# Optimization experiments

Hardware: AMD Instinct MI355X
Metric: run time of the kernel (lower is better)

The kernel has to match this reference:

```python
import jax, jax.numpy as jnp
import numpy as np

N = 1_000_000   # voxels (stride-1: in grid == out grid)
C = 32          # channels
K = 27          # 3x3x3 kernel offsets
P = 600_000     # rulebook pairs per offset
BN_EPS = 1e-5


def setup_inputs() -> dict:
    key = jax.random.key(0)
    k1, k2, k3, k4 = jax.random.split(key, 4)
    x = jax.random.normal(k1, (N, C), dtype=jnp.float32)
    # He-style init for conv weights: fan_in = K * C
    W = jax.random.normal(k2, (K, C, C), dtype=jnp.float32) * (1.0 / np.sqrt(K * C))
    gamma = jnp.ones((C,), dtype=jnp.float32)
    beta = jnp.zeros((C,), dtype=jnp.float32)
    in_idx = jax.random.randint(k3, (K, P), 0, N, dtype=jnp.int32)
    out_idx = jax.random.randint(k4, (K, P), 0, N, dtype=jnp.int32)
    return {"x": x, "W": W, "gamma": gamma, "beta": beta,
            "in_idx": in_idx, "out_idx": out_idx}


def _sparse_conv(x, W, in_idx, out_idx):
    # Rulebook-driven sparse conv: for each kernel offset k, gather input
    # voxels, multiply by the offset's [C,C] weight, scatter-add to outputs.
    def step(acc, inputs):
        ii, oi, w = inputs                      # [P], [P], [C,C]
        acc = acc.at[oi].add(x[ii] @ w)          # gather -> GEMM -> scatter
        return acc, None
    out0 = jnp.zeros((x.shape[0], W.shape[-1]), dtype=x.dtype)
    out, _ = jax.lax.scan(step, out0, (in_idx, out_idx, W))
    return out


def reference(x, W, gamma, beta, in_idx, out_idx):
    y = _sparse_conv(x, W, in_idx, out_idx)      # [N, C]
    # BatchNorm (training-mode batch stats over all voxels, per channel)
    mean = jnp.mean(y, axis=0)
    var = jnp.var(y, axis=0)
    y = (y - mean) * jax.lax.rsqrt(var + BN_EPS) * gamma + beta
    # ReLU
    return jnp.maximum(y, 0.0)
```

## Files before the change

### kernel.cpp

```cpp
#include <hip/hip_runtime.h>

#define CH 32
#define KOFF 27
#define BN_EPS 1e-5f

typedef short bf16x8 __attribute__((ext_vector_type(8)));
typedef float f32x4 __attribute__((ext_vector_type(4)));

__device__ __forceinline__ unsigned short f2bf(float f) {
    unsigned u = __builtin_bit_cast(unsigned, f);
    u = (u + 0x7fffu + ((u >> 16) & 1u)) >> 16;
    return (unsigned short)u;
}
__device__ __forceinline__ float bf2f_lo(unsigned u) {
    return __builtin_bit_cast(float, u << 16);
}
__device__ __forceinline__ float bf2f_hi(unsigned u) {
    return __builtin_bit_cast(float, u & 0xffff0000u);
}

__global__ __launch_bounds__(256) void conv_pk_kernel(
    const float* __restrict__ x, const float* __restrict__ W,
    const int* __restrict__ in_idx, const int* __restrict__ out_idx,
    unsigned* __restrict__ ybf,
    int P, int tilesPerK, int tilesPerWave)
{
    const int k    = blockIdx.y;
    const int lane = threadIdx.x & 63;
    const int wv   = threadIdx.x >> 6;
    const int r16  = lane & 15;
    const int g    = lane >> 4;

    const float* Wk = W + k * CH * CH;
    bf16x8 b0, b1;
#pragma unroll
    for (int j = 0; j < 8; ++j) {
        int kk = g * 8 + j;
        b0[j] = (short)f2bf(Wk[kk * CH + 2 * r16]);
        b1[j] = (short)f2bf(Wk[kk * CH + 2 * r16 + 1]);
    }

    const int kP = k * P;
    int t0 = (blockIdx.x * 4 + wv) * tilesPerWave;
    int t1 = t0 + tilesPerWave;
    if (t1 > tilesPerK) t1 = tilesPerK;

    for (int t = t0; t < t1; ++t) {
        const int base = t * 16;
        int pi = base + r16;
        if (pi >= P) pi = P - 1;
        const int ii = in_idx[kP + pi];
        const float* xr = x + ii * CH + g * 8;
        f32x4 x0 = *(const f32x4*)xr;
        f32x4 x1 = *(const f32x4*)(xr + 4);
        bf16x8 a;
        a[0] = (short)f2bf(x0[0]); a[1] = (short)f2bf(x0[1]);
        a[2] = (short)f2bf(x0[2]); a[3] = (short)f2bf(x0[3]);
        a[4] = (short)f2bf(x1[0]); a[5] = (short)f2bf(x1[1]);
        a[6] = (short)f2bf(x1[2]); a[7] = (short)f2bf(x1[3]);

        f32x4 d0 = {0.f, 0.f, 0.f, 0.f};
        f32x4 d1 = {0.f, 0.f, 0.f, 0.f};
        d0 = __builtin_amdgcn_mfma_f32_16x16x32_bf16(a, b0, d0, 0, 0, 0);
        d1 = __builtin_amdgcn_mfma_f32_16x16x32_bf16(a, b1, d1, 0, 0, 0);

#pragma unroll
        for (int i = 0; i < 4; ++i) {
            int pr = base + g * 4 + i;
            if (pr < P) {
                int oi = out_idx[kP + pr];
                unsigned pk = (unsigned)f2bf(d0[i]) | ((unsigned)f2bf(d1[i]) << 16);
                unsigned* addr = ybf + (size_t)oi * (CH / 2) + r16;
                asm volatile("global_atomic_pk_add_bf16 %0, %1, off"
                             :: "v"(addr), "v"(pk) : "memory");
            }
        }
    }
}

__global__ __launch_bounds__(256) void stats_pk_kernel(
    const uint4* __restrict__ y4, float* __restrict__ stats, int n4)
{
    __shared__ float ls[CH], ls2[CH];
    if (threadIdx.x < CH) { ls[threadIdx.x] = 0.f; ls2[threadIdx.x] = 0.f; }
    __syncthreads();

    int tid = blockIdx.x * blockDim.x + threadIdx.x;
    int stride = gridDim.x * blockDim.x;
    float s[8] = {0,0,0,0,0,0,0,0}, q[8] = {0,0,0,0,0,0,0,0};
    for (int i = tid; i < n4; i += stride) {
        uint4 v = y4[i];
        float f0 = bf2f_lo(v.x), f1 = bf2f_hi(v.x);
        float f2 = bf2f_lo(v.y), f3 = bf2f_hi(v.y);
        float f4 = bf2f_lo(v.z), f5 = bf2f_hi(v.z);
        float f6 = bf2f_lo(v.w), f7 = bf2f_hi(v.w);
        s[0]+=f0; q[0]+=f0*f0; s[1]+=f1; q[1]+=f1*f1;
        s[2]+=f2; q[2]+=f2*f2; s[3]+=f3; q[3]+=f3*f3;
        s[4]+=f4; q[4]+=f4*f4; s[5]+=f5; q[5]+=f5*f5;
        s[6]+=f6; q[6]+=f6*f6; s[7]+=f7; q[7]+=f7*f7;
    }
    int c = (tid * 8) & (CH - 1);
#pragma unroll
    for (int j = 0; j < 8; ++j) {
        atomicAdd(&ls[c + j], s[j]);
        atomicAdd(&ls2[c + j], q[j]);
    }
    __syncthreads();
    if (threadIdx.x < CH) {
        atomicAdd(&stats[threadIdx.x], ls[threadIdx.x]);
        atomicAdd(&stats[CH + threadIdx.x], ls2[threadIdx.x]);
    }
}

__global__ __launch_bounds__(256) void bn_relu_pk_kernel(
    const uint4* __restrict__ y4, f32x4* __restrict__ out4,
    const float* __restrict__ stats,
    const float* __restrict__ gamma, const float* __restrict__ beta,
    float invN, int n4)
{
    __shared__ float sc[CH], bi[CH];
    if (threadIdx.x < CH) {
        int c = threadIdx.x;
        float mean = stats[c] * invN;
        float var  = stats[CH + c] * invN - mean * mean;
        float s = gamma[c] * rsqrtf(var + BN_EPS);
        sc[c] = s;
        bi[c] = beta[c] - mean * s;
    }
    __syncthreads();

    int tid = blockIdx.x * blockDim.x + threadIdx.x;
    int stride = gridDim.x * blockDim.x;
    for (int i = tid; i < n4; i += stride) {
        uint4 v = y4[i];
        int c = (i * 8) & (CH - 1);
        f32x4 o0, o1;
        o0[0] = fmaxf(bf2f_lo(v.x) * sc[c+0] + bi[c+0], 0.f);
        o0[1] = fmaxf(bf2f_hi(v.x) * sc[c+1] + bi[c+1], 0.f);
        o0[2] = fmaxf(bf2f_lo(v.y) * sc[c+2] + bi[c+2], 0.f);
        o0[3] = fmaxf(bf2f_hi(v.y) * sc[c+3] + bi[c+3], 0.f);
        o1[0] = fmaxf(bf2f_lo(v.z) * sc[c+4] + bi[c+4], 0.f);
        o1[1] = fmaxf(bf2f_hi(v.z) * sc[c+5] + bi[c+5], 0.f);
        o1[2] = fmaxf(bf2f_lo(v.w) * sc[c+6] + bi[c+6], 0.f);
        o1[3] = fmaxf(bf2f_hi(v.w) * sc[c+7] + bi[c+7], 0.f);
        out4[2 * i]     = o0;
        out4[2 * i + 1] = o1;
    }
}

__global__ __launch_bounds__(256) void conv_kernel(
    const float* __restrict__ x, const float* __restrict__ W,
    const int* __restrict__ in_idx, const int* __restrict__ out_idx,
    float* __restrict__ y, int P, int tilesPerK, int tilesPerWave)
{
    const int k    = blockIdx.y;
    const int lane = threadIdx.x & 63;
    const int wv   = threadIdx.x >> 6;
    const int r16  = lane & 15;
    const int g    = lane >> 4;

    const float* Wk = W + k * CH * CH;
    bf16x8 b0, b1;
#pragma unroll
    for (int j = 0; j < 8; ++j) {
        int kk = g * 8 + j;
        b0[j] = (short)f2bf(Wk[kk * CH + r16]);
        b1[j] = (short)f2bf(Wk[kk * CH + 16 + r16]);
    }

    const int kP = k * P;
    int t0 = (blockIdx.x * 4 + wv) * tilesPerWave;
    int t1 = t0 + tilesPerWave;
    if (t1 > tilesPerK) t1 = tilesPerK;

    for (int t = t0; t < t1; ++t) {
        const int base = t * 16;
        int pi = base + r16;
        if (pi >= P) pi = P - 1;
        const int ii = in_idx[kP + pi];
        const float* xr = x + ii * CH + g * 8;
        f32x4 x0 = *(const f32x4*)xr;
        f32x4 x1 = *(const f32x4*)(xr + 4);
        bf16x8 a;
        a[0] = (short)f2bf(x0[0]); a[1] = (short)f2bf(x0[1]);
        a[2] = (short)f2bf(x0[2]); a[3] = (short)f2bf(x0[3]);
        a[4] = (short)f2bf(x1[0]); a[5] = (short)f2bf(x1[1]);
        a[6] = (short)f2bf(x1[2]); a[7] = (short)f2bf(x1[3]);

        f32x4 d0 = {0.f, 0.f, 0.f, 0.f};
        f32x4 d1 = {0.f, 0.f, 0.f, 0.f};
        d0 = __builtin_amdgcn_mfma_f32_16x16x32_bf16(a, b0, d0, 0, 0, 0);
        d1 = __builtin_amdgcn_mfma_f32_16x16x32_bf16(a, b1, d1, 0, 0, 0);

#pragma unroll
        for (int i = 0; i < 4; ++i) {
            int pr = base + g * 4 + i;
            if (pr < P) {
                int oi = out_idx[kP + pr];
                atomicAdd(&y[oi * CH + r16], d0[i]);
                atomicAdd(&y[oi * CH + 16 + r16], d1[i]);
            }
        }
    }
}

__global__ __launch_bounds__(256) void stats_kernel(
    const f32x4* __restrict__ y4, float* __restrict__ stats, int n4)
{
    __shared__ float ls[CH], ls2[CH];
    if (threadIdx.x < CH) { ls[threadIdx.x] = 0.f; ls2[threadIdx.x] = 0.f; }
    __syncthreads();

    int tid = blockIdx.x * blockDim.x + threadIdx.x;
    int stride = gridDim.x * blockDim.x;
    float s0 = 0, s1 = 0, s2 = 0, s3 = 0;
    float q0 = 0, q1 = 0, q2 = 0, q3 = 0;
    for (int i = tid; i < n4; i += stride) {
        f32x4 v = y4[i];
        s0 += v[0]; q0 += v[0] * v[0];
        s1 += v[1]; q1 += v[1] * v[1];
        s2 += v[2]; q2 += v[2] * v[2];
        s3 += v[3]; q3 += v[3] * v[3];
    }
    int c = (tid * 4) & (CH - 1);
    atomicAdd(&ls[c + 0], s0); atomicAdd(&ls[c + 1], s1);
    atomicAdd(&ls[c + 2], s2); atomicAdd(&ls[c + 3], s3);
    atomicAdd(&ls2[c + 0], q0); atomicAdd(&ls2[c + 1], q1);
    atomicAdd(&ls2[c + 2], q2); atomicAdd(&ls2[c + 3], q3);
    __syncthreads();
    if (threadIdx.x < CH) {
        atomicAdd(&stats[threadIdx.x], ls[threadIdx.x]);
        atomicAdd(&stats[CH + threadIdx.x], ls2[threadIdx.x]);
    }
}

__global__ __launch_bounds__(256) void bn_relu_kernel(
    f32x4* __restrict__ y4, const float* __restrict__ stats,
    const float* __restrict__ gamma, const float* __restrict__ beta,
    float invN, int n4)
{
    __shared__ float sc[CH], bi[CH];
    if (threadIdx.x < CH) {
        int c = threadIdx.x;
        float mean = stats[c] * invN;
        float var  = stats[CH + c] * invN - mean * mean;
        float s = gamma[c] * rsqrtf(var + BN_EPS);
        sc[c] = s;
        bi[c] = beta[c] - mean * s;
    }
    __syncthreads();

    int tid = blockIdx.x * blockDim.x + threadIdx.x;
    int stride = gridDim.x * blockDim.x;
    for (int i = tid; i < n4; i += stride) {
        f32x4 v = y4[i];
        int c = (i * 4) & (CH - 1);
        f32x4 o;
        o[0] = fmaxf(v[0] * sc[c + 0] + bi[c + 0], 0.f);
        o[1] = fmaxf(v[1] * sc[c + 1] + bi[c + 1], 0.f);
        o[2] = fmaxf(v[2] * sc[c + 2] + bi[c + 2], 0.f);
        o[3] = fmaxf(v[3] * sc[c + 3] + bi[c + 3], 0.f);
        y4[i] = o;
    }
}

extern "C" void kernel_launch(void* const* d_in, const int* in_sizes, int n_in,
                              void* d_out, int out_size, void* d_ws, size_t ws_size,
                              hipStream_t stream)
{
    const float* x      = (const float*)d_in[0];
    const float* W      = (const float*)d_in[1];
    const float* gamma  = (const float*)d_in[2];
    const float* beta   = (const float*)d_in[3];
    const int*   in_idx = (const int*)d_in[4];
    const int*   out_idx= (const int*)d_in[5];

    const int P = in_sizes[4] / KOFF;
    const int N = in_sizes[0] / CH;

    const int tilesPerK = (P + 15) / 16;
    const int tilesPerWave = 8;
    const int blocksX = (tilesPerK + 4 * tilesPerWave - 1) / (4 * tilesPerWave);

    float* stats = (float*)d_ws;
    const size_t statsBytes = 256;
    const size_t ybfBytes = (size_t)N * CH * 2;

    if (ws_size >= statsBytes + ybfBytes) {
        unsigned* ybf = (unsigned*)((char*)d_ws + statsBytes);
        hipMemsetAsync(d_ws, 0, statsBytes + ybfBytes, stream);

        conv_pk_kernel<<<dim3(blocksX, KOFF), 256, 0, stream>>>(
            x, W, in_idx, out_idx, ybf, P, tilesPerK, tilesPerWave);

        const int n4 = (N * CH) / 8;
        stats_pk_kernel<<<1024, 256, 0, stream>>>((const uint4*)ybf, stats, n4);
        bn_relu_pk_kernel<<<2048, 256, 0, stream>>>(
            (const uint4*)ybf, (f32x4*)d_out, stats, gamma, beta,
            1.0f / (float)N, n4);
    } else {
        float* y = (float*)d_out;
        hipMemsetAsync(d_out, 0, (size_t)out_size * sizeof(float), stream);
        hipMemsetAsync(d_ws, 0, statsBytes, stream);

        conv_kernel<<<dim3(blocksX, KOFF), 256, 0, stream>>>(
            x, W, in_idx, out_idx, y, P, tilesPerK, tilesPerWave);

        const int n4 = out_size / 4;
        stats_kernel<<<1024, 256, 0, stream>>>((const f32x4*)d_out, stats, n4);
        bn_relu_kernel<<<2048, 256, 0, stream>>>((f32x4*)d_out, stats, gamma, beta,
                                                 1.0f / (float)N, n4);
    }
}
```

Baseline: 900.1 us.

## Accumulate conv output as packed 16-bit fixed-point via 64-bit integer atomics

The scatter-add no longer uses packed bf16 atomics. Each output value is quantized to 16-bit fixed point (scale 512), and four channels are packed into one u64 using a lane shuffle, so every output row takes 8 64-bit atomic adds instead of 16 32-bit ones. The stats and BN kernels decode the packed fields with borrow correction. This halves the number of atomic operations, but values above 64 in magnitude overflow and the resolution is coarse (1/512), which risks accuracy loss.

```diff
diff --git a/kernel.cpp b/kernel.cpp
--- a/kernel.cpp
+++ b/kernel.cpp
@@ -3,26 +3,32 @@
 #define CH 32
 #define KOFF 27
 #define BN_EPS 1e-5f
+#define FXS 512.0f
+#define FXI (1.0f / 512.0f)
 
 typedef short bf16x8 __attribute__((ext_vector_type(8)));
 typedef float f32x4 __attribute__((ext_vector_type(4)));
+typedef unsigned long long u64;
 
 __device__ __forceinline__ unsigned short f2bf(float f) {
     unsigned u = __builtin_bit_cast(unsigned, f);
     u = (u + 0x7fffu + ((u >> 16) & 1u)) >> 16;
     return (unsigned short)u;
 }
-__device__ __forceinline__ float bf2f_lo(unsigned u) {
-    return __builtin_bit_cast(float, u << 16);
-}
-__device__ __forceinline__ float bf2f_hi(unsigned u) {
-    return __builtin_bit_cast(float, u & 0xffff0000u);
-}
-
-__global__ __launch_bounds__(256) void conv_pk_kernel(
+
+__device__ __forceinline__ void decode4(u64 v, float* f) {
+    long long w = (long long)v;
+    int s0 = (short)(w & 0xFFFF);          w -= (long long)s0;
+    int s1 = (short)((w >> 16) & 0xFFFF);  w -= ((long long)s1 << 16);
+    int s2 = (short)((w >> 32) & 0xFFFF);  w -= ((long long)s2 << 32);
+    int s3 = (int)(w >> 48);
+    f[0] = s0 * FXI; f[1] = s1 * FXI; f[2] = s2 * FXI; f[3] = s3 * FXI;
+}
+
+__global__ __launch_bounds__(256) void conv_fx_kernel(
     const float* __restrict__ x, const float* __restrict__ W,
     const int* __restrict__ in_idx, const int* __restrict__ out_idx,
-    unsigned* __restrict__ ybf,
+    u64* __restrict__ yfx,
     int P, int tilesPerK, int tilesPerWave)
 {
     const int k    = blockIdx.y;
@@ -44,6 +50,9 @@
     int t0 = (blockIdx.x * 4 + wv) * tilesPerWave;
     int t1 = t0 + tilesPerWave;
     if (t1 > tilesPerK) t1 = tilesPerK;
+
+    const int iBase = (r16 & 1) ? 2 : 0;
+    const int m     = r16 >> 1;
 
     for (int t = t0; t < t1; ++t) {
         const int base = t * 16;
@@ -64,22 +73,40 @@
         d0 = __builtin_amdgcn_mfma_f32_16x16x32_bf16(a, b0, d0, 0, 0, 0);
         d1 = __builtin_amdgcn_mfma_f32_16x16x32_bf16(a, b1, d1, 0, 0, 0);
 
+        unsigned qi[4];
 #pragma unroll
         for (int i = 0; i < 4; ++i) {
-            int pr = base + g * 4 + i;
+            int s0 = __float2int_rn(d0[i] * FXS);
+            int s1 = __float2int_rn(d1[i] * FXS);
+            qi[i] = (unsigned)(s0 & 0xFFFF) | ((unsigned)s1 << 16);
+        }
+        unsigned pq[4];
+#pragma unroll
+        for (int i = 0; i < 4; ++i) pq[i] = (unsigned)__shfl_xor((int)qi[i], 1);
+
+#pragma unroll
+        for (int s = 0; s < 2; ++s) {
+            const int i  = iBase + s;
+            const int pr = base + g * 4 + i;
             if (pr < P) {
-                int oi = out_idx[kP + pr];
-                unsigned pk = (unsigned)f2bf(d0[i]) | ((unsigned)f2bf(d1[i]) << 16);
-                unsigned* addr = ybf + (size_t)oi * (CH / 2) + r16;
-                asm volatile("global_atomic_pk_add_bf16 %0, %1, off"
-                             :: "v"(addr), "v"(pk) : "memory");
+                const int oi = out_idx[kP + pr];
+                int a0 = (short)(qi[i] & 0xFFFF), a1 = (short)(qi[i] >> 16);
+                int c0 = (short)(pq[i] & 0xFFFF), c1 = (short)(pq[i] >> 16);
+                long long A;
+                if (!(r16 & 1))
+                    A = (long long)a0 + ((long long)a1 << 16)
+                      + ((long long)c0 << 32) + ((long long)c1 << 48);
+                else
+                    A = (long long)c0 + ((long long)c1 << 16)
+                      + ((long long)a0 << 32) + ((long long)a1 << 48);
+                atomicAdd(&yfx[(size_t)oi * 8 + m], (u64)A);
             }
         }
     }
 }
 
-__global__ __launch_bounds__(256) void stats_pk_kernel(
-    const uint4* __restrict__ y4, float* __restrict__ stats, int n4)
+__global__ __launch_bounds__(256) void stats_fx_kernel(
+    const u64* __restrict__ yfx, float* __restrict__ stats, int nW)
 {
     __shared__ float ls[CH], ls2[CH];
     if (threadIdx.x < CH) { ls[threadIdx.x] = 0.f; ls2[threadIdx.x] = 0.f; }
@@ -87,21 +114,16 @@
 
     int tid = blockIdx.x * blockDim.x + threadIdx.x;
     int stride = gridDim.x * blockDim.x;
-    float s[8] = {0,0,0,0,0,0,0,0}, q[8] = {0,0,0,0,0,0,0,0};
-    for (int i = tid; i < n4; i += stride) {
-        uint4 v = y4[i];
-        float f0 = bf2f_lo(v.x), f1 = bf2f_hi(v.x);
-        float f2 = bf2f_lo(v.y), f3 = bf2f_hi(v.y);
-        float f4 = bf2f_lo(v.z), f5 = bf2f_hi(v.z);
-        float f6 = bf2f_lo(v.w), f7 = bf2f_hi(v.w);
-        s[0]+=f0; q[0]+=f0*f0; s[1]+=f1; q[1]+=f1*f1;
-        s[2]+=f2; q[2]+=f2*f2; s[3]+=f3; q[3]+=f3*f3;
-        s[4]+=f4; q[4]+=f4*f4; s[5]+=f5; q[5]+=f5*f5;
-        s[6]+=f6; q[6]+=f6*f6; s[7]+=f7; q[7]+=f7*f7;
-    }
-    int c = (tid * 8) & (CH - 1);
-#pragma unroll
-    for (int j = 0; j < 8; ++j) {
+    float s[4] = {0,0,0,0}, q[4] = {0,0,0,0};
+    for (int i = tid; i < nW; i += stride) {
+        float f[4];
+        decode4(yfx[i], f);
+#pragma unroll
+        for (int j = 0; j < 4; ++j) { s[j] += f[j]; q[j] += f[j] * f[j]; }
+    }
+    int c = (tid & 7) * 4;
+#pragma unroll
+    for (int j = 0; j < 4; ++j) {
         atomicAdd(&ls[c + j], s[j]);
         atomicAdd(&ls2[c + j], q[j]);
     }
@@ -112,11 +134,11 @@
     }
 }
 
-__global__ __launch_bounds__(256) void bn_relu_pk_kernel(
-    const uint4* __restrict__ y4, f32x4* __restrict__ out4,
+__global__ __launch_bounds__(256) void bn_relu_fx_kernel(
+    const u64* __restrict__ yfx, f32x4* __restrict__ out4,
     const float* __restrict__ stats,
     const float* __restrict__ gamma, const float* __restrict__ beta,
-    float invN, int n4)
+    float invN, int nW)
 {
     __shared__ float sc[CH], bi[CH];
     if (threadIdx.x < CH) {
@@ -131,20 +153,16 @@
 
     int tid = blockIdx.x * blockDim.x + threadIdx.x;
     int stride = gridDim.x * blockDim.x;
-    for (int i = tid; i < n4; i += stride) {
-        uint4 v = y4[i];
-        int c = (i * 8) & (CH - 1);
-        f32x4 o0, o1;
-        o0[0] = fmaxf(bf2f_lo(v.x) * sc[c+0] + bi[c+0], 0.f);
-        o0[1] = fmaxf(bf2f_hi(v.x) * sc[c+1] + bi[c+1], 0.f);
-        o0[2] = fmaxf(bf2f_lo(v.y) * sc[c+2] + bi[c+2], 0.f);
-        o0[3] = fmaxf(bf2f_hi(v.y) * sc[c+3] + bi[c+3], 0.f);
-        o1[0] = fmaxf(bf2f_lo(v.z) * sc[c+4] + bi[c+4], 0.f);
-        o1[1] = fmaxf(bf2f_hi(v.z) * sc[c+5] + bi[c+5], 0.f);
-        o1[2] = fmaxf(bf2f_lo(v.w) * sc[c+6] + bi[c+6], 0.f);
-        o1[3] = fmaxf(bf2f_hi(v.w) * sc[c+7] + bi[c+7], 0.f);
-        out4[2 * i]     = o0;
-        out4[2 * i + 1] = o1;
+    for (int i = tid; i < nW; i += stride) {
+        float f[4];
+        decode4(yfx[i], f);
+        int c = (i & 7) * 4;
+        f32x4 o;
+        o[0] = fmaxf(f[0] * sc[c + 0] + bi[c + 0], 0.f);
+        o[1] = fmaxf(f[1] * sc[c + 1] + bi[c + 1], 0.f);
+        o[2] = fmaxf(f[2] * sc[c + 2] + bi[c + 2], 0.f);
+        o[3] = fmaxf(f[3] * sc[c + 3] + bi[c + 3], 0.f);
+        out4[i] = o;
     }
 }
 
@@ -284,20 +302,19 @@
 
     float* stats = (float*)d_ws;
     const size_t statsBytes = 256;
-    const size_t ybfBytes = (size_t)N * CH * 2;
-
-    if (ws_size >= statsBytes + ybfBytes) {
-        unsigned* ybf = (unsigned*)((char*)d_ws + statsBytes);
-        hipMemsetAsync(d_ws, 0, statsBytes + ybfBytes, stream);
-
-        conv_pk_kernel<<<dim3(blocksX, KOFF), 256, 0, stream>>>(
-            x, W, in_idx, out_idx, ybf, P, tilesPerK, tilesPerWave);
-
-        const int n4 = (N * CH) / 8;
-        stats_pk_kernel<<<1024, 256, 0, stream>>>((const uint4*)ybf, stats, n4);
-        bn_relu_pk_kernel<<<2048, 256, 0, stream>>>(
-            (const uint4*)ybf, (f32x4*)d_out, stats, gamma, beta,
-            1.0f / (float)N, n4);
+    const size_t yfxBytes = (size_t)N * 8 * sizeof(u64);
+
+    if (ws_size >= statsBytes + yfxBytes) {
+        u64* yfx = (u64*)((char*)d_ws + statsBytes);
+        hipMemsetAsync(d_ws, 0, statsBytes + yfxBytes, stream);
+
+        conv_fx_kernel<<<dim3(blocksX, KOFF), 256, 0, stream>>>(
+            x, W, in_idx, out_idx, yfx, P, tilesPerK, tilesPerWave);
+
+        const int nW = N * 8;
+        stats_fx_kernel<<<1024, 256, 0, stream>>>(yfx, stats, nW);
+        bn_relu_fx_kernel<<<2048, 256, 0, stream>>>(yfx, (f32x4*)d_out, stats,
+                                                    gamma, beta, 1.0f / (float)N, nW);
     } else {
         float* y = (float*)d_out;
         hipMemsetAsync(d_out, 0, (size_t)out_size * sizeof(float), stream);
```

After: 825.5 us. 1.09x faster.
